# Performance work log

Hardware: AMD Instinct MI355X
Metric: run time of the kernel (lower is better)

## Reference

```python
import jax, jax.numpy as jnp
import numpy as np

D_MODEL = 1024
NUM_HEAD = 16
D_HEAD = D_MODEL // NUM_HEAD
NEG_INF = -1e9


def setup_inputs() -> dict:
    key = jax.random.key(0)
    ks = jax.random.split(key, 10)
    B, S = 16, 512
    v = jax.random.normal(ks[0], (B, S, D_MODEL), dtype=jnp.float32)
    lengths = jax.random.randint(ks[1], (B,), 1, S + 1, dtype=jnp.int32)
    scale = 0.02
    Wq = jax.random.normal(ks[2], (D_MODEL, D_MODEL), dtype=jnp.float32) * scale
    bq = jnp.zeros((D_MODEL,), dtype=jnp.float32)
    Wk = jax.random.normal(ks[3], (D_MODEL, D_MODEL), dtype=jnp.float32) * scale
    bk = jnp.zeros((D_MODEL,), dtype=jnp.float32)
    Wv = jax.random.normal(ks[4], (D_MODEL, D_MODEL), dtype=jnp.float32) * scale
    bv = jnp.zeros((D_MODEL,), dtype=jnp.float32)
    Wo = jax.random.normal(ks[5], (D_MODEL, D_MODEL), dtype=jnp.float32) * scale
    bo = jnp.zeros((D_MODEL,), dtype=jnp.float32)
    return {"v": v, "lengths": lengths, "Wq": Wq, "bq": bq, "Wk": Wk,
            "bk": bk, "Wv": Wv, "bv": bv, "Wo": Wo, "bo": bo}


def reference(v, lengths, Wq, bq, Wk, bk, Wv, bv, Wo, bo):
    B, S, D = v.shape
    H, Dh = NUM_HEAD, D_HEAD
    # key-padding mask: True where key position j is valid (j < lengths[b])
    valid = jnp.arange(S)[None, :] < lengths[:, None]          # [B, S]
    # project q, k, v and split heads -> [B, H, S, Dh]
    def split_heads(x):
        return x.reshape(B, S, H, Dh).transpose(0, 2, 1, 3)
    q = split_heads(v @ Wq + bq)
    k = split_heads(v @ Wk + bk)
    val = split_heads(v @ Wv + bv)
    scores = jnp.einsum('bhqd,bhkd->bhqk', q, k) / jnp.sqrt(jnp.float32(Dh))
    scores = jnp.where(valid[:, None, None, :], scores, NEG_INF)  # mask padded keys
    attn = jax.nn.softmax(scores, axis=-1)
    out = jnp.einsum('bhqk,bhkd->bhqd', attn, val)              # [B, H, S, Dh]
    out = out.transpose(0, 2, 1, 3).reshape(B, S, D)
    return out @ Wo + bo
```

## Files before the change

kernel.cpp:

```cpp
#include <hip/hip_runtime.h>
#include <hip/hip_bf16.h>

typedef unsigned short u16;
typedef unsigned int u32;
typedef __attribute__((ext_vector_type(8))) short short8;
typedef __attribute__((ext_vector_type(4))) float f32x4;
typedef __attribute__((ext_vector_type(4))) unsigned int u32x4;

#define B_SZ 16
#define S_SZ 512
#define D_SZ 1024
#define H_SZ 16
#define DH_SZ 64
#define M_SZ (B_SZ * S_SZ)
#define EXPSCALE 0.18033688f

__device__ __forceinline__ void gload_lds16(const void* g, void* l) {
  __builtin_amdgcn_global_load_lds(
      (const __attribute__((address_space(1))) unsigned int*)g,
      (__attribute__((address_space(3))) unsigned int*)l,
      16, 0, 0);
}

__device__ __forceinline__ u16 bf16b(float x) {
  __hip_bfloat16 h = __float2bfloat16(x);
  return *(u16*)&h;
}

__global__ __launch_bounds__(256) void prep(
    const float* __restrict__ v, u16* __restrict__ vB,
    const float* __restrict__ W0, const float* __restrict__ W1,
    const float* __restrict__ W2, const float* __restrict__ W3,
    u16* __restrict__ T0, u16* __restrict__ T1,
    u16* __restrict__ T2, u16* __restrict__ T3) {
  __shared__ float tile[32][33];
  const int bid = blockIdx.x;
  if (bid < 8192) {
    int i = bid * 256 + threadIdx.x;
    const float4 f = *(const float4*)&v[(size_t)i * 4];
    ushort4 o;
    o.x = bf16b(f.x); o.y = bf16b(f.y); o.z = bf16b(f.z); o.w = bf16b(f.w);
    *(ushort4*)&vB[(size_t)i * 4] = o;
    return;
  }
  const int tb = bid - 8192;
  const int z = tb >> 10, rem = tb & 1023;
  const int by = rem >> 5, bx = rem & 31;
  const float* W; u16* T;
  switch (z) {
    case 0: W = W0; T = T0; break;
    case 1: W = W1; T = T1; break;
    case 2: W = W2; T = T2; break;
    default: W = W3; T = T3; break;
  }
  int tx = threadIdx.x & 31, ty = threadIdx.x >> 5;
  int x = bx * 32 + tx;
#pragma unroll
  for (int i = 0; i < 32; i += 8)
    tile[ty + i][tx] = W[(size_t)(by * 32 + ty + i) * 1024 + x];
  __syncthreads();
  int x2 = by * 32 + tx;
#pragma unroll
  for (int i = 0; i < 32; i += 8)
    T[(size_t)(bx * 32 + ty + i) * 1024 + x2] = bf16b(tile[tx][ty + i]);
}

struct G8 {
  const u16* A; const u16* Bt;
  u16* As; u16* Bs;
  int m0, n0;
  int wave, c, quad, r7, wm, wn;
  int srow, slc8;
};

#define AS_T (128 * 64)
#define BS_T (256 * 64)

__device__ __forceinline__ void stage_a(const G8& g, int buf, int kt, int i) {
  const int grp = g.wave * 2 + i;
  gload_lds16(&g.A[(size_t)(g.m0 + grp * 8 + g.srow) * 1024 + kt * 64 + g.slc8],
              g.As + buf * AS_T + grp * 512);
}
__device__ __forceinline__ void stage_b(const G8& g, int buf, int kt, int i) {
  const int grp = g.wave * 4 + i;
  gload_lds16(&g.Bt[(size_t)(g.n0 + grp * 8 + g.srow) * 1024 + kt * 64 + g.slc8],
              g.Bs + buf * BS_T + grp * 512);
}

template<bool ST, int VM>
__device__ __forceinline__ void tile_step(const G8& g, int cur, int stg, int kt2,
                                          f32x4 acc[4][4]) {
  const u16* ab = g.As + cur * AS_T;
  const u16* bb = g.Bs + cur * BS_T;
  short8 af[4], bf[4];

  {
    const int pc = (g.quad ^ g.r7) * 8;
#pragma unroll
    for (int i = 0; i < 4; ++i) {
      af[i] = *(const short8*)&ab[(g.wm + i * 16 + g.c) * 64 + pc];
      bf[i] = *(const short8*)&bb[(g.wn + i * 16 + g.c) * 64 + pc];
    }
    if constexpr (ST) {
      stage_a(g, stg, kt2, 0);
      stage_a(g, stg, kt2, 1);
      stage_b(g, stg, kt2, 0);
    }
    __builtin_amdgcn_s_barrier();
    __builtin_amdgcn_s_setprio(1);
#pragma unroll
    for (int mi = 0; mi < 4; ++mi)
#pragma unroll
      for (int ni = 0; ni < 4; ++ni)
        acc[mi][ni] = __builtin_amdgcn_mfma_f32_16x16x32_bf16(
            af[mi], bf[ni], acc[mi][ni], 0, 0, 0);
    __builtin_amdgcn_s_setprio(0);
    __builtin_amdgcn_s_barrier();
  }

  {
    const int pc = ((4 + g.quad) ^ g.r7) * 8;
#pragma unroll
    for (int i = 0; i < 4; ++i) {
      af[i] = *(const short8*)&ab[(g.wm + i * 16 + g.c) * 64 + pc];
      bf[i] = *(const short8*)&bb[(g.wn + i * 16 + g.c) * 64 + pc];
    }
    if constexpr (ST) {
      stage_b(g, stg, kt2, 1);
      stage_b(g, stg, kt2, 2);
      stage_b(g, stg, kt2, 3);
    }
    __builtin_amdgcn_s_barrier();
    __builtin_amdgcn_s_setprio(1);
#pragma unroll
    for (int mi = 0; mi < 4; ++mi)
#pragma unroll
      for (int ni = 0; ni < 4; ++ni)
        acc[mi][ni] = __builtin_amdgcn_mfma_f32_16x16x32_bf16(
            af[mi], bf[ni], acc[mi][ni], 0, 0, 0);
    __builtin_amdgcn_s_setprio(0);
    if constexpr (VM == 6) {
      asm volatile("s_waitcnt vmcnt(6)" ::: "memory");
      __builtin_amdgcn_s_barrier();
    } else if constexpr (VM == 0) {
      asm volatile("s_waitcnt vmcnt(0)" ::: "memory");
      __builtin_amdgcn_s_barrier();
    }
  }
}

__device__ __forceinline__ void gemm_core8(
    const u16* __restrict__ A, const u16* __restrict__ Bt,
    u16* AsB, u16* BsB, int m0, int n0, f32x4 acc[4][4]) {
  const int tid = threadIdx.x;
  const int lane = tid & 63;
  G8 g;
  g.A = A; g.Bt = Bt; g.As = AsB; g.Bs = BsB;
  g.m0 = m0; g.n0 = n0;
  g.wave = tid >> 6;
  g.c = lane & 15; g.quad = lane >> 4; g.r7 = g.c & 7;
  g.wm = (g.wave >> 2) * 64;
  g.wn = (g.wave & 3) * 64;
  g.srow = lane >> 3;
  g.slc8 = ((lane & 7) ^ g.srow) * 8;

  stage_a(g, 0, 0, 0); stage_a(g, 0, 0, 1);
  stage_b(g, 0, 0, 0); stage_b(g, 0, 0, 1); stage_b(g, 0, 0, 2); stage_b(g, 0, 0, 3);
  stage_a(g, 1, 1, 0); stage_a(g, 1, 1, 1);
  stage_b(g, 1, 1, 0); stage_b(g, 1, 1, 1); stage_b(g, 1, 1, 2); stage_b(g, 1, 1, 3);
  asm volatile("s_waitcnt vmcnt(6)" ::: "memory");
  __builtin_amdgcn_s_barrier();

  int cur = 0, stg = 2;
#pragma unroll 1
  for (int t = 0; t < 14; ++t) {
    tile_step<true, 6>(g, cur, stg, t + 2, acc);
    cur = (cur == 2) ? 0 : cur + 1;
    stg = (stg == 2) ? 0 : stg + 1;
  }
  tile_step<false, 0>(g, cur, 0, 0, acc);
  tile_step<false, -1>(g, 0, 0, 0, acc);
}

template<int Z>
__global__ __launch_bounds__(512, 2) void gemm_split(
    const u16* __restrict__ A, const u16* __restrict__ Bt,
    const float* __restrict__ bias, u16* __restrict__ Out) {
  __shared__ u16 As[3][AS_T];
  __shared__ u16 Bs[3][BS_T];
  const int m0 = blockIdx.x * 128, n0 = blockIdx.y * 256;

  f32x4 acc[4][4];
#pragma unroll
  for (int i = 0; i < 4; ++i)
#pragma unroll
    for (int j = 0; j < 4; ++j) acc[i][j] = f32x4{0.f, 0.f, 0.f, 0.f};

  gemm_core8(A, Bt, &As[0][0], &Bs[0][0], m0, n0, acc);

  const int lane = threadIdx.x & 63, wave = threadIdx.x >> 6;
  const int wm = (wave >> 2) * 64, wn = (wave & 3) * 64;
  const int c = lane & 15, quad = lane >> 4;
#pragma unroll
  for (int ni = 0; ni < 4; ++ni) {
    int n = n0 + wn + ni * 16 + c;
    float bval = bias[n];
#pragma unroll
    for (int mi = 0; mi < 4; ++mi) {
      int mb = m0 + wm + mi * 16 + quad * 4;
      if constexpr (Z == 2) {
        int bb = mb >> 9, s = mb & 511, hh = n >> 6, d = n & 63;
        ushort4 st;
        st.x = bf16b(acc[mi][ni][0] + bval);
        st.y = bf16b(acc[mi][ni][1] + bval);
        st.z = bf16b(acc[mi][ni][2] + bval);
        st.w = bf16b(acc[mi][ni][3] + bval);
        *(ushort4*)&Out[(((size_t)(bb * 16 + hh) * 64 + d) << 9) + s] = st;
      } else {
#pragma unroll
        for (int r = 0; r < 4; ++r) {
          int m = mb + r;
          float val = acc[mi][ni][r] + bval;
          if constexpr (Z == 0) val *= EXPSCALE;
          if constexpr (Z == 0) {
            Out[(size_t)m * 1024 + n] = bf16b(val);
          } else {
            int bb = m >> 9, s = m & 511, hh = n >> 6, d = n & 63;
            Out[(((size_t)(bb * 16 + hh) * 512 + s) << 6) + d] = bf16b(val);
          }
        }
      }
    }
  }
}

__global__ __launch_bounds__(512, 2) void gemm_out(
    const u16* __restrict__ A, const u16* __restrict__ Bt,
    const float* __restrict__ bias, float* __restrict__ Cf) {
  __shared__ u16 As[3][AS_T];
  __shared__ u16 Bs[3][BS_T];
  const int m0 = blockIdx.x * 128, n0 = blockIdx.y * 256;

  f32x4 acc[4][4];
#pragma unroll
  for (int i = 0; i < 4; ++i)
#pragma unroll
    for (int j = 0; j < 4; ++j) acc[i][j] = f32x4{0.f, 0.f, 0.f, 0.f};

  gemm_core8(A, Bt, &As[0][0], &Bs[0][0], m0, n0, acc);

  const int lane = threadIdx.x & 63, wave = threadIdx.x >> 6;
  const int wm = (wave >> 2) * 64, wn = (wave & 3) * 64;
  const int c = lane & 15, quad = lane >> 4;
#pragma unroll
  for (int ni = 0; ni < 4; ++ni) {
    int n = n0 + wn + ni * 16 + c;
    float bval = bias[n];
#pragma unroll
    for (int mi = 0; mi < 4; ++mi) {
#pragma unroll
      for (int r = 0; r < 4; ++r) {
        int m = m0 + wm + mi * 16 + quad * 4 + r;
        Cf[(size_t)m * 1024 + n] = acc[mi][ni][r] + bval;
      }
    }
  }
}

__global__ __launch_bounds__(256) void attn_v9(
    const u16* __restrict__ Q, const u16* __restrict__ Kt,
    const u16* __restrict__ Vt, const int* __restrict__ lengths,
    u16* __restrict__ O) {
  const int qc = blockIdx.x, h = blockIdx.y, b = blockIdx.z;
  const int t = threadIdx.x;
  const int lane = t & 63, wave = t >> 6;
  const int c = lane & 15, quad = lane >> 4;
  const int len = lengths[b];
  const int q0 = qc * 128 + wave * 32;

  __shared__ __align__(16) u16 Ks[64 * 64];
  __shared__ __align__(16) u16 Vs[64 * 64];

  const size_t bBase = (size_t)b * (S_SZ * D_SZ);
  const size_t hBase = ((size_t)(b * H_SZ + h)) * (S_SZ * DH_SZ);

  short8 aq[2][2];
#pragma unroll
  for (int qt = 0; qt < 2; ++qt) {
    aq[qt][0] = *(const short8*)&Q[bBase + (size_t)(q0 + qt * 16 + c) * 1024 + h * 64 + quad * 8];
    aq[qt][1] = *(const short8*)&Q[bBase + (size_t)(q0 + qt * 16 + c) * 1024 + h * 64 + 32 + quad * 8];
  }

  const short ONE = (short)0x3F80;
  const short8 ones = {ONE, ONE, ONE, ONE, ONE, ONE, ONE, ONE};

  const int srow = lane >> 3;
  const int slc = (lane & 7) ^ srow;

  f32x4 o[2][4];
  f32x4 osum[2];
#pragma unroll
  for (int qt = 0; qt < 2; ++qt) {
    osum[qt] = f32x4{0.f, 0.f, 0.f, 0.f};
#pragma unroll
    for (int i = 0; i < 4; ++i) o[qt][i] = f32x4{0.f, 0.f, 0.f, 0.f};
  }

  const int kmax = (len + 63) & ~63;
  for (int k0 = 0; k0 < kmax; k0 += 64) {
    __syncthreads();
#pragma unroll
    for (int g = 0; g < 2; ++g) {
      const int grp = wave * 2 + g;
      const int rho = grp * 8 + srow;
      const int grow = ((rho >> 4) & 1) * 32 + ((rho >> 2) & 3) * 8 +
                       ((rho >> 5) & 1) * 4 + (rho & 3);
      gload_lds16(&Kt[hBase + (size_t)(k0 + grow) * 64 + slc * 8],
                  &Ks[grp * 512]);
      gload_lds16(&Vt[hBase + (size_t)(grp * 8 + srow) * 512 + k0 + slc * 8],
                  &Vs[grp * 512]);
    }
    __syncthreads();

    const bool full = (k0 + 64 <= len);

#pragma unroll
    for (int half = 0; half < 2; ++half) {
      u32 pk[2][4];
#pragma unroll
      for (int ss = 0; ss < 2; ++ss) {
        const int sub = half + ss * 2;
        const int row = sub * 16 + c;
        short8 bk0 = *(const short8*)&Ks[row * 64 + ((quad ^ (c & 7))) * 8];
        short8 bk1 = *(const short8*)&Ks[row * 64 + (((4 + quad) ^ (c & 7))) * 8];
        const int keyb = k0 + (sub & 1) * 32 + quad * 8 + (sub >> 1) * 4;
#pragma unroll
        for (int qt = 0; qt < 2; ++qt) {
          f32x4 s = {0.f, 0.f, 0.f, 0.f};
          s = __builtin_amdgcn_mfma_f32_16x16x32_bf16(bk0, aq[qt][0], s, 0, 0, 0);
          s = __builtin_amdgcn_mfma_f32_16x16x32_bf16(bk1, aq[qt][1], s, 0, 0, 0);
          float p0, p1, p2, p3;
          if (full) {
            p0 = exp2f(s[0]); p1 = exp2f(s[1]);
            p2 = exp2f(s[2]); p3 = exp2f(s[3]);
          } else {
            p0 = (keyb + 0) < len ? exp2f(s[0]) : 0.f;
            p1 = (keyb + 1) < len ? exp2f(s[1]) : 0.f;
            p2 = (keyb + 2) < len ? exp2f(s[2]) : 0.f;
            p3 = (keyb + 3) < len ? exp2f(s[3]) : 0.f;
          }
          pk[qt][ss * 2 + 0] = (u32)bf16b(p0) | ((u32)bf16b(p1) << 16);
          pk[qt][ss * 2 + 1] = (u32)bf16b(p2) | ((u32)bf16b(p3) << 16);
        }
      }
      u32x4 w0 = {pk[0][0], pk[0][1], pk[0][2], pk[0][3]};
      u32x4 w1 = {pk[1][0], pk[1][1], pk[1][2], pk[1][3]};
      short8 pa0, pa1;
      __builtin_memcpy(&pa0, &w0, 16);
      __builtin_memcpy(&pa1, &w1, 16);
      osum[0] = __builtin_amdgcn_mfma_f32_16x16x32_bf16(pa0, ones, osum[0], 0, 0, 0);
      osum[1] = __builtin_amdgcn_mfma_f32_16x16x32_bf16(pa1, ones, osum[1], 0, 0, 0);
#pragma unroll
      for (int dt = 0; dt < 4; ++dt) {
        const int vrow = dt * 16 + c;
        short8 vb = *(const short8*)&Vs[vrow * 64 + (((half * 4 + quad) ^ (c & 7))) * 8];
        o[0][dt] = __builtin_amdgcn_mfma_f32_16x16x32_bf16(pa0, vb, o[0][dt], 0, 0, 0);
        o[1][dt] = __builtin_amdgcn_mfma_f32_16x16x32_bf16(pa1, vb, o[1][dt], 0, 0, 0);
      }
    }
  }

#pragma unroll
  for (int qt = 0; qt < 2; ++qt) {
    float inv[4];
#pragma unroll
    for (int r = 0; r < 4; ++r) inv[r] = 1.0f / osum[qt][r];
#pragma unroll
    for (int dt = 0; dt < 4; ++dt) {
#pragma unroll
      for (int r = 0; r < 4; ++r) {
        int s = q0 + qt * 16 + quad * 4 + r;
        float val = o[qt][dt][r] * inv[r];
        O[bBase + (size_t)s * 1024 + h * 64 + dt * 16 + c] = bf16b(val);
      }
    }
  }
}

extern "C" void kernel_launch(void* const* d_in, const int* in_sizes, int n_in,
                              void* d_out, int out_size, void* d_ws, size_t ws_size,
                              hipStream_t stream) {
  const float* v  = (const float*)d_in[0];
  const int* lengths = (const int*)d_in[1];
  const float* Wq = (const float*)d_in[2];
  const float* bq = (const float*)d_in[3];
  const float* Wk = (const float*)d_in[4];
  const float* bk = (const float*)d_in[5];
  const float* Wv = (const float*)d_in[6];
  const float* bv = (const float*)d_in[7];
  const float* Wo = (const float*)d_in[8];
  const float* bo = (const float*)d_in[9];

  char* ws = (char*)d_ws;
  const size_t TSZ = (size_t)M_SZ * D_SZ * 2;
  const size_t WSZ = (size_t)1 << 21;
  u16* vB  = (u16*)(ws);
  u16* AO  = vB;
  u16* WqT = (u16*)(ws + TSZ + 0 * WSZ);
  u16* WkT = (u16*)(ws + TSZ + 1 * WSZ);
  u16* WvT = (u16*)(ws + TSZ + 2 * WSZ);
  u16* WoT = (u16*)(ws + TSZ + 3 * WSZ);
  u16* Qb  = (u16*)(ws + TSZ + 4 * WSZ + 0 * TSZ);
  u16* Kt  = (u16*)(ws + TSZ + 4 * WSZ + 1 * TSZ);
  u16* Vt  = (u16*)(ws + TSZ + 4 * WSZ + 2 * TSZ);

  prep<<<dim3(8192 + 4096), 256, 0, stream>>>(v, vB, Wq, Wk, Wv, Wo, WqT, WkT, WvT, WoT);

  gemm_split<0><<<dim3(64, 4), 512, 0, stream>>>(vB, WqT, bq, Qb);
  gemm_split<1><<<dim3(64, 4), 512, 0, stream>>>(vB, WkT, bk, Kt);
  gemm_split<2><<<dim3(64, 4), 512, 0, stream>>>(vB, WvT, bv, Vt);

  attn_v9<<<dim3(4, 16, 16), 256, 0, stream>>>(Qb, Kt, Vt, lengths, AO);

  gemm_out<<<dim3(64, 4), 512, 0, stream>>>(AO, WoT, bo, (float*)d_out);
}
```

Measured before the change: 225.9 us.

## Merge QKV projections into one launch and halve attention query tile per block

The three separate Q/K/V projection GEMM launches become one launch with a z grid dimension that picks weights, bias and output layout per block. This gives 768 blocks instead of three waves of 256 and removes launch gaps. The attention kernel now gives each wave 16 queries instead of 32, doubling the block count to 2048 for better occupancy and load balance across variable lengths. In exchange, each K/V tile loaded to LDS is reused by half as many queries, which doubles K/V global traffic, and the epilogue now branches at runtime on z.

Measured after the change: 222.6 us. Within noise of the previous version (-1.5%).

```diff
diff --git a/kernel.cpp b/kernel.cpp
--- a/kernel.cpp
+++ b/kernel.cpp
@@ -182,12 +182,16 @@
   tile_step<false, -1>(g, 0, 0, 0, acc);
 }
 
-template<int Z>
-__global__ __launch_bounds__(512, 2) void gemm_split(
-    const u16* __restrict__ A, const u16* __restrict__ Bt,
-    const float* __restrict__ bias, u16* __restrict__ Out) {
+__global__ __launch_bounds__(512, 2) void gemm_qkv(
+    const u16* __restrict__ A,
+    const u16* __restrict__ BtQ, const u16* __restrict__ BtK, const u16* __restrict__ BtV,
+    const float* __restrict__ bq, const float* __restrict__ bk, const float* __restrict__ bv,
+    u16* __restrict__ Qo, u16* __restrict__ Kt, u16* __restrict__ Vt) {
   __shared__ u16 As[3][AS_T];
   __shared__ u16 Bs[3][BS_T];
+  const int z = blockIdx.z;
+  const u16* Bt = (z == 0) ? BtQ : (z == 1) ? BtK : BtV;
+  const float* bias = (z == 0) ? bq : (z == 1) ? bk : bv;
   const int m0 = blockIdx.x * 128, n0 = blockIdx.y * 256;
 
   f32x4 acc[4][4];
@@ -208,26 +212,26 @@
 #pragma unroll
     for (int mi = 0; mi < 4; ++mi) {
       int mb = m0 + wm + mi * 16 + quad * 4;
-      if constexpr (Z == 2) {
+      if (z == 2) {
         int bb = mb >> 9, s = mb & 511, hh = n >> 6, d = n & 63;
         ushort4 st;
         st.x = bf16b(acc[mi][ni][0] + bval);
         st.y = bf16b(acc[mi][ni][1] + bval);
         st.z = bf16b(acc[mi][ni][2] + bval);
         st.w = bf16b(acc[mi][ni][3] + bval);
-        *(ushort4*)&Out[(((size_t)(bb * 16 + hh) * 64 + d) << 9) + s] = st;
-      } else {
+        *(ushort4*)&Vt[(((size_t)(bb * 16 + hh) * 64 + d) << 9) + s] = st;
+      } else if (z == 0) {
 #pragma unroll
         for (int r = 0; r < 4; ++r) {
           int m = mb + r;
-          float val = acc[mi][ni][r] + bval;
-          if constexpr (Z == 0) val *= EXPSCALE;
-          if constexpr (Z == 0) {
-            Out[(size_t)m * 1024 + n] = bf16b(val);
-          } else {
-            int bb = m >> 9, s = m & 511, hh = n >> 6, d = n & 63;
-            Out[(((size_t)(bb * 16 + hh) * 512 + s) << 6) + d] = bf16b(val);
-          }
+          Qo[(size_t)m * 1024 + n] = bf16b((acc[mi][ni][r] + bval) * EXPSCALE);
+        }
+      } else {
+#pragma unroll
+        for (int r = 0; r < 4; ++r) {
+          int m = mb + r;
+          int bb = m >> 9, s = m & 511, hh = n >> 6, d = n & 63;
+          Kt[(((size_t)(bb * 16 + hh) * 512 + s) << 6) + d] = bf16b(acc[mi][ni][r] + bval);
         }
       }
     }
@@ -267,7 +271,7 @@
   }
 }
 
-__global__ __launch_bounds__(256) void attn_v9(
+__global__ __launch_bounds__(256) void attn_v10(
     const u16* __restrict__ Q, const u16* __restrict__ Kt,
     const u16* __restrict__ Vt, const int* __restrict__ lengths,
     u16* __restrict__ O) {
@@ -276,7 +280,7 @@
   const int lane = t & 63, wave = t >> 6;
   const int c = lane & 15, quad = lane >> 4;
   const int len = lengths[b];
-  const int q0 = qc * 128 + wave * 32;
+  const int q0 = qc * 64 + wave * 16;
 
   __shared__ __align__(16) u16 Ks[64 * 64];
   __shared__ __align__(16) u16 Vs[64 * 64];
@@ -284,12 +288,8 @@
   const size_t bBase = (size_t)b * (S_SZ * D_SZ);
   const size_t hBase = ((size_t)(b * H_SZ + h)) * (S_SZ * DH_SZ);
 
-  short8 aq[2][2];
-#pragma unroll
-  for (int qt = 0; qt < 2; ++qt) {
-    aq[qt][0] = *(const short8*)&Q[bBase + (size_t)(q0 + qt * 16 + c) * 1024 + h * 64 + quad * 8];
-    aq[qt][1] = *(const short8*)&Q[bBase + (size_t)(q0 + qt * 16 + c) * 1024 + h * 64 + 32 + quad * 8];
-  }
+  short8 aq0 = *(const short8*)&Q[bBase + (size_t)(q0 + c) * 1024 + h * 64 + quad * 8];
+  short8 aq1 = *(const short8*)&Q[bBase + (size_t)(q0 + c) * 1024 + h * 64 + 32 + quad * 8];
 
   const short ONE = (short)0x3F80;
   const short8 ones = {ONE, ONE, ONE, ONE, ONE, ONE, ONE, ONE};
@@ -297,14 +297,10 @@
   const int srow = lane >> 3;
   const int slc = (lane & 7) ^ srow;
 
-  f32x4 o[2][4];
-  f32x4 osum[2];
-#pragma unroll
-  for (int qt = 0; qt < 2; ++qt) {
-    osum[qt] = f32x4{0.f, 0.f, 0.f, 0.f};
-#pragma unroll
-    for (int i = 0; i < 4; ++i) o[qt][i] = f32x4{0.f, 0.f, 0.f, 0.f};
-  }
+  f32x4 o[4];
+  f32x4 osum = {0.f, 0.f, 0.f, 0.f};
+#pragma unroll
+  for (int i = 0; i < 4; ++i) o[i] = f32x4{0.f, 0.f, 0.f, 0.f};
 
   const int kmax = (len + 63) & ~63;
   for (int k0 = 0; k0 < kmax; k0 += 64) {
@@ -326,7 +322,7 @@
 
 #pragma unroll
     for (int half = 0; half < 2; ++half) {
-      u32 pk[2][4];
+      u32 pk[4];
 #pragma unroll
       for (int ss = 0; ss < 2; ++ss) {
         const int sub = half + ss * 2;
@@ -334,55 +330,45 @@
         short8 bk0 = *(const short8*)&Ks[row * 64 + ((quad ^ (c & 7))) * 8];
         short8 bk1 = *(const short8*)&Ks[row * 64 + (((4 + quad) ^ (c & 7))) * 8];
         const int keyb = k0 + (sub & 1) * 32 + quad * 8 + (sub >> 1) * 4;
-#pragma unroll
-        for (int qt = 0; qt < 2; ++qt) {
-          f32x4 s = {0.f, 0.f, 0.f, 0.f};
-          s = __builtin_amdgcn_mfma_f32_16x16x32_bf16(bk0, aq[qt][0], s, 0, 0, 0);
-          s = __builtin_amdgcn_mfma_f32_16x16x32_bf16(bk1, aq[qt][1], s, 0, 0, 0);
-          float p0, p1, p2, p3;
-          if (full) {
-            p0 = exp2f(s[0]); p1 = exp2f(s[1]);
-            p2 = exp2f(s[2]); p3 = exp2f(s[3]);
-          } else {
-            p0 = (keyb + 0) < len ? exp2f(s[0]) : 0.f;
-            p1 = (keyb + 1) < len ? exp2f(s[1]) : 0.f;
-            p2 = (keyb + 2) < len ? exp2f(s[2]) : 0.f;
-            p3 = (keyb + 3) < len ? exp2f(s[3]) : 0.f;
-          }
-          pk[qt][ss * 2 + 0] = (u32)bf16b(p0) | ((u32)bf16b(p1) << 16);
-          pk[qt][ss * 2 + 1] = (u32)bf16b(p2) | ((u32)bf16b(p3) << 16);
+        f32x4 s = {0.f, 0.f, 0.f, 0.f};
+        s = __builtin_amdgcn_mfma_f32_16x16x32_bf16(bk0, aq0, s, 0, 0, 0);
+        s = __builtin_amdgcn_mfma_f32_16x16x32_bf16(bk1, aq1, s, 0, 0, 0);
+        float p0, p1, p2, p3;
+        if (full) {
+          p0 = exp2f(s[0]); p1 = exp2f(s[1]);
+          p2 = exp2f(s[2]); p3 = exp2f(s[3]);
+        } else {
+          p0 = (keyb + 0) < len ? exp2f(s[0]) : 0.f;
+          p1 = (keyb + 1) < len ? exp2f(s[1]) : 0.f;
+          p2 = (keyb + 2) < len ? exp2f(s[2]) : 0.f;
+          p3 = (keyb + 3) < len ? exp2f(s[3]) : 0.f;
         }
+        pk[ss * 2 + 0] = (u32)bf16b(p0) | ((u32)bf16b(p1) << 16);
+        pk[ss * 2 + 1] = (u32)bf16b(p2) | ((u32)bf16b(p3) << 16);
       }
-      u32x4 w0 = {pk[0][0], pk[0][1], pk[0][2], pk[0][3]};
-      u32x4 w1 = {pk[1][0], pk[1][1], pk[1][2], pk[1][3]};
-      short8 pa0, pa1;
-      __builtin_memcpy(&pa0, &w0, 16);
-      __builtin_memcpy(&pa1, &w1, 16);
-      osum[0] = __builtin_amdgcn_mfma_f32_16x16x32_bf16(pa0, ones, osum[0], 0, 0, 0);
-      osum[1] = __builtin_amdgcn_mfma_f32_16x16x32_bf16(pa1, ones, osum[1], 0, 0, 0);
+      u32x4 w0 = {pk[0], pk[1], pk[2], pk[3]};
+      short8 pa;
+      __builtin_memcpy(&pa, &w0, 16);
+      osum = __builtin_amdgcn_mfma_f32_16x16x32_bf16(pa, ones, osum, 0, 0, 0);
 #pragma unroll
       for (int dt = 0; dt < 4; ++dt) {
         const int vrow = dt * 16 + c;
         short8 vb = *(const short8*)&Vs[vrow * 64 + (((half * 4 + quad) ^ (c & 7))) * 8];
-        o[0][dt] = __builtin_amdgcn_mfma_f32_16x16x32_bf16(pa0, vb, o[0][dt], 0, 0, 0);
-        o[1][dt] = __builtin_amdgcn_mfma_f32_16x16x32_bf16(pa1, vb, o[1][dt], 0, 0, 0);
+        o[dt] = __builtin_amdgcn_mfma_f32_16x16x32_bf16(pa, vb, o[dt], 0, 0, 0);
       }
     }
   }
 
-#pragma unroll
-  for (int qt = 0; qt < 2; ++qt) {
-    float inv[4];
-#pragma unroll
-    for (int r = 0; r < 4; ++r) inv[r] = 1.0f / osum[qt][r];
-#pragma unroll
-    for (int dt = 0; dt < 4; ++dt) {
-#pragma unroll
-      for (int r = 0; r < 4; ++r) {
-        int s = q0 + qt * 16 + quad * 4 + r;
-        float val = o[qt][dt][r] * inv[r];
-        O[bBase + (size_t)s * 1024 + h * 64 + dt * 16 + c] = bf16b(val);
-      }
+  float inv[4];
+#pragma unroll
+  for (int r = 0; r < 4; ++r) inv[r] = 1.0f / osum[r];
+#pragma unroll
+  for (int dt = 0; dt < 4; ++dt) {
+#pragma unroll
+    for (int r = 0; r < 4; ++r) {
+      int s = q0 + quad * 4 + r;
+      float val = o[dt][r] * inv[r];
+      O[bBase + (size_t)s * 1024 + h * 64 + dt * 16 + c] = bf16b(val);
     }
   }
 }
@@ -416,11 +402,9 @@
 
   prep<<<dim3(8192 + 4096), 256, 0, stream>>>(v, vB, Wq, Wk, Wv, Wo, WqT, WkT, WvT, WoT);
 
-  gemm_split<0><<<dim3(64, 4), 512, 0, stream>>>(vB, WqT, bq, Qb);
-  gemm_split<1><<<dim3(64, 4), 512, 0, stream>>>(vB, WkT, bk, Kt);
-  gemm_split<2><<<dim3(64, 4), 512, 0, stream>>>(vB, WvT, bv, Vt);
-
-  attn_v9<<<dim3(4, 16, 16), 256, 0, stream>>>(Qb, Kt, Vt, lengths, AO);
+  gemm_qkv<<<dim3(64, 4, 3), 512, 0, stream>>>(vB, WqT, WkT, WvT, bq, bk, bv, Qb, Kt, Vt);
+
+  attn_v10<<<dim3(8, 16, 16), 256, 0, stream>>>(Qb, Kt, Vt, lengths, AO);
 
   gemm_out<<<dim3(64, 4), 512, 0, stream>>>(AO, WoT, bo, (float*)d_out);
 }
```
